# Optimization experiments

Measured on AMD Instinct MI355X. Metric: run time of the kernel, lower is better.

Reference implementation:

```python
import jax, jax.numpy as jnp
import numpy as np

B = 65536       # batch (rollout particles)
H = 5           # history_steps
F = 50          # forward_steps
DT = 0.01


def setup_inputs() -> dict:
    key = jax.random.key(0)
    k0, k1, k2, k3, k4, k5 = jax.random.split(key, 6)
    full_states = jax.random.uniform(k0, (B, H, 8), jnp.float32, 0.1, 1.0)
    actions = jax.random.uniform(k1, (B, F, 2), jnp.float32, 0.0, 0.5)
    fc1_w = jax.random.normal(k2, (16, 5 * H), jnp.float32) * 0.1
    fc1_b = jax.random.normal(k3, (16,), jnp.float32) * 0.1
    fc2_w = jax.random.normal(k4, (3, 16), jnp.float32) * 0.1
    fc2_b = jax.random.normal(k5, (3,), jnp.float32) * 0.1
    # [lf, lr, m_div_Iz, cm1, cm2, cr, cd, tire_B, tire_C, tire_D]
    params = jnp.array([0.09 - 0.036, 0.036, 0.05 * 12.0 / 0.02,
                        7.0, 0.1, 0.24 * 7.0, 0.1,
                        10.0, 0.1, (180.0 / np.pi) / 10.0 / 0.1], jnp.float32)
    return {"full_states": full_states, "actions": actions,
            "fc1_w": fc1_w, "fc1_b": fc1_b, "fc2_w": fc2_w, "fc2_b": fc2_b,
            "params": params, "enable_rnn": 1}


def reference(full_states, actions, fc1_w, fc1_b, fc2_w, fc2_b, params, enable_rnn):
    lf, lr, m_div_Iz = params[0], params[1], params[2]
    cm1, cm2, cr, cd = params[3], params[4], params[5], params[6]
    tB, tC, tD = params[7], params[8], params[9]
    bounds = jnp.array([5.0, 5.0, 3.0], full_states.dtype)
    dt = jnp.asarray(DT, full_states.dtype)
    pi = jnp.asarray(np.pi, full_states.dtype)

    def tire(slip):  # Pacejka magic formula
        return tD * jnp.sin(tC * jnp.arctan(tB * slip))

    def step(window, action):
        # window: [B, H, 8] rolling history of full states; action: [B, 2]
        latest = window[:, -1, :]
        throttle, steering = latest[:, 6], latest[:, 7]
        psi = latest[:, 4]
        c, s = jnp.cos(psi), jnp.sin(psi)
        # world -> body frame velocities (omega forced to 0 as in source)
        Vx = latest[:, 1] * c + latest[:, 3] * s
        Vy = -latest[:, 1] * s + latest[:, 3] * c
        slip_f = -jnp.arctan(Vy / Vx) + steering
        slip_r = jnp.arctan(-Vy / Vx)
        laf, lar = tire(slip_f), tire(slip_r)
        fwd_acc = (cm1 - cm2 * Vx) * throttle - cr - cd * Vx * Vx
        Vx = Vx + (fwd_acc - laf * jnp.sin(steering)) * dt
        Vy = Vy + (lar + laf * jnp.cos(steering)) * dt
        omega = m_div_Iz * (laf * lf * jnp.cos(steering) - lar * lr) * dt
        if enable_rnn:
            ph = window[:, :, 4]
            ch, sh = jnp.cos(ph), jnp.sin(ph)
            Vxh = window[:, :, 1] * ch + window[:, :, 3] * sh
            Vyh = -window[:, :, 1] * sh + window[:, :, 3] * ch
            # stack order matches torch.stack([Vx,Vy,omega,throttle,steering],dim=1).view(B,-1)
            feat = jnp.concatenate([Vxh, Vyh, window[:, :, 5],
                                    window[:, :, 6], window[:, :, 7]], axis=1)  # [B, 5H]
            y1 = jnp.tanh(feat @ fc1_w.T + fc1_b)
            y2 = jnp.tanh(y1 @ fc2_w.T + fc2_b) * bounds
            Vx = Vx + y2[:, 0] * dt
            Vy = Vy + y2[:, 1] * dt
            omega = omega + y2[:, 2] * dt
        # body -> world frame
        Vxg = Vx * c - Vy * s
        Vyg = Vx * s + Vy * c
        psi_new = jnp.mod(psi + omega * dt + pi, 2 * pi) - pi
        new_state = jnp.stack([latest[:, 0] + Vxg * dt, Vxg,
                               latest[:, 2] + Vyg * dt, Vyg,
                               psi_new, omega], axis=1)          # [B, 6]
        new_full = jnp.concatenate([new_state, action], axis=1)   # [B, 8]
        window = jnp.concatenate([window[:, 1:], new_full[:, None]], axis=1)
        return window, new_full

    _, outs = jax.lax.scan(step, full_states, jnp.swapaxes(actions, 0, 1))
    return jnp.swapaxes(outs, 0, 1)  # [B, F, 8] = future_states
```

## Files before the change

### kernel.cpp

```cpp
#include <hip/hip_runtime.h>
#include <hip/hip_fp16.h>
#include <math.h>


__device__ __forceinline__ float rfl(float x) {
    return __int_as_float(__builtin_amdgcn_readfirstlane(__float_as_int(x)));
}

__device__ __forceinline__ float mixlo(unsigned int w, float f, float acc) {
    float d;
    asm("v_fma_mix_f32 %0, %1, %2, %3 op_sel:[0,0,0] op_sel_hi:[1,0,0]"
        : "=v"(d) : "v"(w), "v"(f), "v"(acc));
    return d;
}
__device__ __forceinline__ float mixhi(unsigned int w, float f, float acc) {
    float d;
    asm("v_fma_mix_f32 %0, %1, %2, %3 op_sel:[1,0,0] op_sel_hi:[1,0,0]"
        : "=v"(d) : "v"(w), "v"(f), "v"(acc));
    return d;
}

__device__ __forceinline__ float fast_tanhf(float x) {
    float e = __builtin_amdgcn_exp2f(x * 2.8853900817779268f);
    return 1.0f - 2.0f * __builtin_amdgcn_rcpf(e + 1.0f);
}

__device__ __forceinline__ float sin_small(float x) {
    float x2 = x * x;
    return x * (1.0f + x2 * (-1.66666667e-1f + x2 * 8.33333338e-3f));
}

__device__ __forceinline__ float fatanf(float x) {
    float ax = fabsf(x);
    bool big = ax > 1.0f;
    float z  = big ? __builtin_amdgcn_rcpf(ax) : ax;
    float z2 = z * z;
    float p = fmaf(z2, -0.0117212f, 0.05265332f);
    p = fmaf(z2, p, -0.11643287f);
    p = fmaf(z2, p,  0.19354346f);
    p = fmaf(z2, p, -0.33262347f);
    p = fmaf(z2, p,  0.99997726f);
    float r = z * p;
    r = big ? (1.57079632679489662f - r) : r;
    return copysignf(r, x);
}

#define FOR_K_TAIL(M) \
    M(1) M(2) M(3) M(4) M(5) M(6) M(7) M(8) M(9) M(10) M(11) M(12) \
    M(13) M(14) M(15) M(16) M(17) M(18) M(19) M(20) M(21) M(22) M(23) M(24)
#define FOR_K_ALL(M) M(0) FOR_K_TAIL(M)

__global__ __launch_bounds__(256)
__attribute__((amdgpu_waves_per_eu(1, 1)))
void sim_kernel(const float* __restrict__ fs,
                const float* __restrict__ act,
                const float* __restrict__ w1,
                const float* __restrict__ b1,
                const float* __restrict__ w2,
                const float* __restrict__ b2,
                const float* __restrict__ prm,
                const int*   __restrict__ rnnp,
                float* __restrict__ out)
{
    __shared__ unsigned int sWH[200];

    const int tid = threadIdx.x;
    if (tid < 200) {
        int k = tid >> 3, j = tid & 7;
        unsigned int lo = (unsigned int)__half_as_ushort(__float2half(w1[(2 * j) * 25 + k]));
        unsigned int hi = (unsigned int)__half_as_ushort(__float2half(w1[(2 * j + 1) * 25 + k]));
        sWH[tid] = lo | (hi << 16);
    }
    __syncthreads();

    const int b = blockIdx.x * 256 + tid;

    const float4* fsp = reinterpret_cast<const float4*>(fs + (size_t)b * 40);
    const float4* ap  = reinterpret_cast<const float4*>(act + (size_t)b * 100);
    float4 acur = ap[0];

    float wf[40];
#pragma unroll
    for (int i = 0; i < 10; ++i) {
        float4 v = fsp[i];
        wf[i * 4 + 0] = v.x; wf[i * 4 + 1] = v.y;
        wf[i * 4 + 2] = v.z; wf[i * 4 + 3] = v.w;
    }

    const float lf = rfl(prm[0]), lr = rfl(prm[1]), mIz = rfl(prm[2]);
    const float cm1 = rfl(prm[3]), cm2 = rfl(prm[4]), cr = rfl(prm[5]);
    const float cd = rfl(prm[6]);
    const float tB = rfl(prm[7]), tC = rfl(prm[8]), tD = rfl(prm[9]);
    const int   rnn = __builtin_amdgcn_readfirstlane(rnnp[0]);
    const float dt = 0.01f;
    const float PI = 3.14159265358979323846f;
    const float INV2PI = 0.15915494309189535f;
    const float TWOPI = 6.28318530717958647692f;

#define DECLW2(K) \
    float w2a_##K = rfl(w2[(K)]);      \
    float w2b_##K = rfl(w2[16 + (K)]); \
    float w2c_##K = rfl(w2[32 + (K)]);
    DECLW2(0) DECLW2(1) DECLW2(2) DECLW2(3)
    DECLW2(4) DECLW2(5) DECLW2(6) DECLW2(7)
    DECLW2(8) DECLW2(9) DECLW2(10) DECLW2(11)
    DECLW2(12) DECLW2(13) DECLW2(14) DECLW2(15)
#undef DECLW2
    const float b2s0 = rfl(b2[0]), b2s1 = rfl(b2[1]), b2s2 = rfl(b2[2]);

#define DECLB1(K) float b1v_##K = b1[(K)];
    DECLB1(0) DECLB1(1) DECLB1(2) DECLB1(3)
    DECLB1(4) DECLB1(5) DECLB1(6) DECLB1(7)
    DECLB1(8) DECLB1(9) DECLB1(10) DECLB1(11)
    DECLB1(12) DECLB1(13) DECLB1(14) DECLB1(15)
#undef DECLB1

    float feat[25];
#pragma unroll
    for (int t = 0; t < 5; ++t) {
        float ph = wf[t * 8 + 4];
        float ch = __cosf(ph), sh = __sinf(ph);
        float v1 = wf[t * 8 + 1], v3 = wf[t * 8 + 3];
        feat[t]      =  v1 * ch + v3 * sh;
        feat[5 + t]  = -v1 * sh + v3 * ch;
        feat[10 + t] = wf[t * 8 + 5];
        feat[15 + t] = wf[t * 8 + 6];
        feat[20 + t] = wf[t * 8 + 7];
    }

    float x   = wf[32];
    float y   = wf[34];
    float psi = wf[36];
    float c = __cosf(psi), s = __sinf(psi);

#define WLOAD(K)                                                             \
    unsigned int wp##K##_0, wp##K##_1, wp##K##_2, wp##K##_3,                 \
                 wp##K##_4, wp##K##_5, wp##K##_6, wp##K##_7;                 \
    {                                                                        \
        const uint4* p = reinterpret_cast<const uint4*>(&sWH[(K) * 8]);      \
        uint4 u0 = p[0], u1 = p[1];                                          \
        wp##K##_0 = u0.x; wp##K##_1 = u0.y;                                  \
        wp##K##_2 = u0.z; wp##K##_3 = u0.w;                                  \
        wp##K##_4 = u1.x; wp##K##_5 = u1.y;                                  \
        wp##K##_6 = u1.z; wp##K##_7 = u1.w;                                  \
    }
    FOR_K_ALL(WLOAD)
#undef WLOAD

    float* outp = out + (size_t)b * 400;

#pragma unroll 1
    for (int f2 = 0; f2 < 25; ++f2) {
        float4 anext = ap[(f2 < 24) ? (f2 + 1) : 24];

#pragma unroll
        for (int half = 0; half < 2; ++half) {
            const float a0 = half ? acur.z : acur.x;
            const float a1 = half ? acur.w : acur.y;

            const float throttle = feat[19];
            const float steering = feat[24];
            const float Vx = feat[4];
            const float Vy = feat[9];

            const float atr    = fatanf(Vy * __builtin_amdgcn_rcpf(Vx));
            const float slip_f = -atr + steering;
            const float slip_r = -atr;
            const float laf = tD * sin_small(tC * fatanf(tB * slip_f));
            const float lar = tD * sin_small(tC * fatanf(tB * slip_r));

            const float st_s = __sinf(steering), st_c = __cosf(steering);
            const float fwd  = (cm1 - cm2 * Vx) * throttle - cr - cd * Vx * Vx;

            float Vx2   = Vx + (fwd - laf * st_s) * dt;
            float Vy2   = Vy + (lar + laf * st_c) * dt;
            float omega = mIz * (laf * lf * st_c - lar * lr) * dt;

            if (rnn) {
                const float f0 = feat[0];
                float y1_0  = mixlo(wp0_0, f0, b1v_0);
                float y1_1  = mixhi(wp0_0, f0, b1v_1);
                float y1_2  = mixlo(wp0_1, f0, b1v_2);
                float y1_3  = mixhi(wp0_1, f0, b1v_3);
                float y1_4  = mixlo(wp0_2, f0, b1v_4);
                float y1_5  = mixhi(wp0_2, f0, b1v_5);
                float y1_6  = mixlo(wp0_3, f0, b1v_6);
                float y1_7  = mixhi(wp0_3, f0, b1v_7);
                float y1_8  = mixlo(wp0_4, f0, b1v_8);
                float y1_9  = mixhi(wp0_4, f0, b1v_9);
                float y1_10 = mixlo(wp0_5, f0, b1v_10);
                float y1_11 = mixhi(wp0_5, f0, b1v_11);
                float y1_12 = mixlo(wp0_6, f0, b1v_12);
                float y1_13 = mixhi(wp0_6, f0, b1v_13);
                float y1_14 = mixlo(wp0_7, f0, b1v_14);
                float y1_15 = mixhi(wp0_7, f0, b1v_15);
#define GK(K)                                        \
                {                                    \
                    const float fk = feat[(K)];      \
                    y1_0  = mixlo(wp##K##_0, fk, y1_0);  \
                    y1_1  = mixhi(wp##K##_0, fk, y1_1);  \
                    y1_2  = mixlo(wp##K##_1, fk, y1_2);  \
                    y1_3  = mixhi(wp##K##_1, fk, y1_3);  \
                    y1_4  = mixlo(wp##K##_2, fk, y1_4);  \
                    y1_5  = mixhi(wp##K##_2, fk, y1_5);  \
                    y1_6  = mixlo(wp##K##_3, fk, y1_6);  \
                    y1_7  = mixhi(wp##K##_3, fk, y1_7);  \
                    y1_8  = mixlo(wp##K##_4, fk, y1_8);  \
                    y1_9  = mixhi(wp##K##_4, fk, y1_9);  \
                    y1_10 = mixlo(wp##K##_5, fk, y1_10); \
                    y1_11 = mixhi(wp##K##_5, fk, y1_11); \
                    y1_12 = mixlo(wp##K##_6, fk, y1_12); \
                    y1_13 = mixhi(wp##K##_6, fk, y1_13); \
                    y1_14 = mixlo(wp##K##_7, fk, y1_14); \
                    y1_15 = mixhi(wp##K##_7, fk, y1_15); \
                }
                FOR_K_TAIL(GK)
#undef GK

                float z0 = b2s0, z1 = b2s1, z2 = b2s2;
#define FC2(K)                                       \
                {                                    \
                    float t_ = fast_tanhf(y1_##K);   \
                    z0 = fmaf(t_, w2a_##K, z0);      \
                    z1 = fmaf(t_, w2b_##K, z1);      \
                    z2 = fmaf(t_, w2c_##K, z2);      \
                }
                FC2(0) FC2(1) FC2(2) FC2(3)
                FC2(4) FC2(5) FC2(6) FC2(7)
                FC2(8) FC2(9) FC2(10) FC2(11)
                FC2(12) FC2(13) FC2(14) FC2(15)
#undef FC2
                Vx2   += fast_tanhf(z0) * 5.0f * dt;
                Vy2   += fast_tanhf(z1) * 5.0f * dt;
                omega += fast_tanhf(z2) * 3.0f * dt;
            }

            const float Vxg = Vx2 * c - Vy2 * s;
            const float Vyg = Vx2 * s + Vy2 * c;
            float pn = psi + omega * dt + PI;
            pn = pn - floorf(pn * INV2PI) * TWOPI - PI;

            x = x + Vxg * dt;
            y = y + Vyg * dt;

            float4 o0 = make_float4(x, Vxg, y, Vyg);
            float4 o1 = make_float4(pn, omega, a0, a1);
            reinterpret_cast<float4*>(outp)[0] = o0;
            reinterpret_cast<float4*>(outp)[1] = o1;
            outp += 8;

            psi = pn;
            c = __cosf(pn);
            s = __sinf(pn);
#pragma unroll
            for (int j = 0; j < 5; ++j)
#pragma unroll
                for (int t = 0; t < 4; ++t)
                    feat[j * 5 + t] = feat[j * 5 + t + 1];
            feat[4]  =  Vxg * c + Vyg * s;
            feat[9]  = -Vxg * s + Vyg * c;
            feat[14] = omega;
            feat[19] = a0;
            feat[24] = a1;
        }
        acur = anext;
    }
}

extern "C" void kernel_launch(void* const* d_in, const int* in_sizes, int n_in,
                              void* d_out, int out_size, void* d_ws, size_t ws_size,
                              hipStream_t stream) {
    const float* fs  = (const float*)d_in[0];
    const float* act = (const float*)d_in[1];
    const float* w1  = (const float*)d_in[2];
    const float* b1  = (const float*)d_in[3];
    const float* w2  = (const float*)d_in[4];
    const float* b2  = (const float*)d_in[5];
    const float* prm = (const float*)d_in[6];
    const int*   rnn = (const int*)d_in[7];
    float* out = (float*)d_out;

    const int Bn = in_sizes[0] / 40;
    dim3 grid(Bn / 256), block(256);
    hipLaunchKernelGGL(sim_kernel, grid, block, 0, stream,
                       fs, act, w1, b1, w2, b2, prm, rnn, out);
}
```

Baseline: 213.5 us.

## Split each car across two lanes, halving MLP hidden units per lane

Each car is now handled by a pair of adjacent lanes. Each lane computes 8 of the 16 hidden units of the first MLP layer and a partial second-layer sum, and the partials are combined with a cross-lane shuffle. Each lane also writes one float4 half of the output row. Both lanes duplicate the scalar physics. The grid doubles, the waves-per-EU hint rises to 2, and the accumulating fma_mix calls now use read-write asm operands. The aim is lower register pressure and more parallelism on the serial rollout, at the cost of redundant physics work and a shuffle every step.

New measurement: 206.8 us. -3.1%, faster.

```diff
diff --git a/kernel.cpp b/kernel.cpp
--- a/kernel.cpp
+++ b/kernel.cpp
@@ -7,16 +7,24 @@
     return __int_as_float(__builtin_amdgcn_readfirstlane(__float_as_int(x)));
 }
 
-__device__ __forceinline__ float mixlo(unsigned int w, float f, float acc) {
+__device__ __forceinline__ void mixlo_acc(float& acc, unsigned int w, float f) {
+    asm("v_fma_mix_f32 %0, %1, %2, %0 op_sel:[0,0,0] op_sel_hi:[1,0,0]"
+        : "+v"(acc) : "v"(w), "v"(f));
+}
+__device__ __forceinline__ void mixhi_acc(float& acc, unsigned int w, float f) {
+    asm("v_fma_mix_f32 %0, %1, %2, %0 op_sel:[1,0,0] op_sel_hi:[1,0,0]"
+        : "+v"(acc) : "v"(w), "v"(f));
+}
+__device__ __forceinline__ float mixlo_init(unsigned int w, float f, float c) {
     float d;
     asm("v_fma_mix_f32 %0, %1, %2, %3 op_sel:[0,0,0] op_sel_hi:[1,0,0]"
-        : "=v"(d) : "v"(w), "v"(f), "v"(acc));
+        : "=v"(d) : "v"(w), "v"(f), "v"(c));
     return d;
 }
-__device__ __forceinline__ float mixhi(unsigned int w, float f, float acc) {
+__device__ __forceinline__ float mixhi_init(unsigned int w, float f, float c) {
     float d;
     asm("v_fma_mix_f32 %0, %1, %2, %3 op_sel:[1,0,0] op_sel_hi:[1,0,0]"
-        : "=v"(d) : "v"(w), "v"(f), "v"(acc));
+        : "=v"(d) : "v"(w), "v"(f), "v"(c));
     return d;
 }
 
@@ -51,7 +59,7 @@
 #define FOR_K_ALL(M) M(0) FOR_K_TAIL(M)
 
 __global__ __launch_bounds__(256)
-__attribute__((amdgpu_waves_per_eu(1, 1)))
+__attribute__((amdgpu_waves_per_eu(2, 2)))
 void sim_kernel(const float* __restrict__ fs,
                 const float* __restrict__ act,
                 const float* __restrict__ w1,
@@ -73,10 +81,12 @@
     }
     __syncthreads();
 
-    const int b = blockIdx.x * 256 + tid;
-
-    const float4* fsp = reinterpret_cast<const float4*>(fs + (size_t)b * 40);
-    const float4* ap  = reinterpret_cast<const float4*>(act + (size_t)b * 100);
+    const int gt  = blockIdx.x * 256 + tid;
+    const int car = gt >> 1;
+    const int h   = gt & 1;
+
+    const float4* fsp = reinterpret_cast<const float4*>(fs + (size_t)car * 40);
+    const float4* ap  = reinterpret_cast<const float4*>(act + (size_t)car * 100);
     float4 acur = ap[0];
 
     float wf[40];
@@ -96,24 +106,32 @@
     const float PI = 3.14159265358979323846f;
     const float INV2PI = 0.15915494309189535f;
     const float TWOPI = 6.28318530717958647692f;
-
-#define DECLW2(K) \
-    float w2a_##K = rfl(w2[(K)]);      \
-    float w2b_##K = rfl(w2[16 + (K)]); \
-    float w2c_##K = rfl(w2[32 + (K)]);
-    DECLW2(0) DECLW2(1) DECLW2(2) DECLW2(3)
-    DECLW2(4) DECLW2(5) DECLW2(6) DECLW2(7)
-    DECLW2(8) DECLW2(9) DECLW2(10) DECLW2(11)
-    DECLW2(12) DECLW2(13) DECLW2(14) DECLW2(15)
-#undef DECLW2
     const float b2s0 = rfl(b2[0]), b2s1 = rfl(b2[1]), b2s2 = rfl(b2[2]);
 
-#define DECLB1(K) float b1v_##K = b1[(K)];
-    DECLB1(0) DECLB1(1) DECLB1(2) DECLB1(3)
-    DECLB1(4) DECLB1(5) DECLB1(6) DECLB1(7)
-    DECLB1(8) DECLB1(9) DECLB1(10) DECLB1(11)
-    DECLB1(12) DECLB1(13) DECLB1(14) DECLB1(15)
-#undef DECLB1
+    float b1v_0, b1v_1, b1v_2, b1v_3, b1v_4, b1v_5, b1v_6, b1v_7;
+    {
+        const float4* p = reinterpret_cast<const float4*>(b1 + 8 * h);
+        float4 u0 = p[0], u1 = p[1];
+        b1v_0 = u0.x; b1v_1 = u0.y; b1v_2 = u0.z; b1v_3 = u0.w;
+        b1v_4 = u1.x; b1v_5 = u1.y; b1v_6 = u1.z; b1v_7 = u1.w;
+    }
+    float w2av_0, w2av_1, w2av_2, w2av_3, w2av_4, w2av_5, w2av_6, w2av_7;
+    float w2bv_0, w2bv_1, w2bv_2, w2bv_3, w2bv_4, w2bv_5, w2bv_6, w2bv_7;
+    float w2cv_0, w2cv_1, w2cv_2, w2cv_3, w2cv_4, w2cv_5, w2cv_6, w2cv_7;
+    {
+        const float4* pa = reinterpret_cast<const float4*>(w2 + 8 * h);
+        float4 a0_ = pa[0], a1_ = pa[1];
+        w2av_0 = a0_.x; w2av_1 = a0_.y; w2av_2 = a0_.z; w2av_3 = a0_.w;
+        w2av_4 = a1_.x; w2av_5 = a1_.y; w2av_6 = a1_.z; w2av_7 = a1_.w;
+        const float4* pb = reinterpret_cast<const float4*>(w2 + 16 + 8 * h);
+        float4 b0_ = pb[0], b1_ = pb[1];
+        w2bv_0 = b0_.x; w2bv_1 = b0_.y; w2bv_2 = b0_.z; w2bv_3 = b0_.w;
+        w2bv_4 = b1_.x; w2bv_5 = b1_.y; w2bv_6 = b1_.z; w2bv_7 = b1_.w;
+        const float4* pc = reinterpret_cast<const float4*>(w2 + 32 + 8 * h);
+        float4 c0_ = pc[0], c1_ = pc[1];
+        w2cv_0 = c0_.x; w2cv_1 = c0_.y; w2cv_2 = c0_.z; w2cv_3 = c0_.w;
+        w2cv_4 = c1_.x; w2cv_5 = c1_.y; w2cv_6 = c1_.z; w2cv_7 = c1_.w;
+    }
 
     float feat[25];
 #pragma unroll
@@ -134,20 +152,17 @@
     float c = __cosf(psi), s = __sinf(psi);
 
 #define WLOAD(K)                                                             \
-    unsigned int wp##K##_0, wp##K##_1, wp##K##_2, wp##K##_3,                 \
-                 wp##K##_4, wp##K##_5, wp##K##_6, wp##K##_7;                 \
+    unsigned int wp##K##_0, wp##K##_1, wp##K##_2, wp##K##_3;                 \
     {                                                                        \
-        const uint4* p = reinterpret_cast<const uint4*>(&sWH[(K) * 8]);      \
-        uint4 u0 = p[0], u1 = p[1];                                          \
-        wp##K##_0 = u0.x; wp##K##_1 = u0.y;                                  \
-        wp##K##_2 = u0.z; wp##K##_3 = u0.w;                                  \
-        wp##K##_4 = u1.x; wp##K##_5 = u1.y;                                  \
-        wp##K##_6 = u1.z; wp##K##_7 = u1.w;                                  \
+        const uint4* p =                                                     \
+            reinterpret_cast<const uint4*>(&sWH[(K) * 8 + 4 * h]);           \
+        uint4 u = *p;                                                        \
+        wp##K##_0 = u.x; wp##K##_1 = u.y; wp##K##_2 = u.z; wp##K##_3 = u.w;  \
     }
     FOR_K_ALL(WLOAD)
 #undef WLOAD
 
-    float* outp = out + (size_t)b * 400;
+    float* outp = out + (size_t)car * 400 + 4 * h;
 
 #pragma unroll 1
     for (int f2 = 0; f2 < 25; ++f2) {
@@ -178,61 +193,47 @@
 
             if (rnn) {
                 const float f0 = feat[0];
-                float y1_0  = mixlo(wp0_0, f0, b1v_0);
-                float y1_1  = mixhi(wp0_0, f0, b1v_1);
-                float y1_2  = mixlo(wp0_1, f0, b1v_2);
-                float y1_3  = mixhi(wp0_1, f0, b1v_3);
-                float y1_4  = mixlo(wp0_2, f0, b1v_4);
-                float y1_5  = mixhi(wp0_2, f0, b1v_5);
-                float y1_6  = mixlo(wp0_3, f0, b1v_6);
-                float y1_7  = mixhi(wp0_3, f0, b1v_7);
-                float y1_8  = mixlo(wp0_4, f0, b1v_8);
-                float y1_9  = mixhi(wp0_4, f0, b1v_9);
-                float y1_10 = mixlo(wp0_5, f0, b1v_10);
-                float y1_11 = mixhi(wp0_5, f0, b1v_11);
-                float y1_12 = mixlo(wp0_6, f0, b1v_12);
-                float y1_13 = mixhi(wp0_6, f0, b1v_13);
-                float y1_14 = mixlo(wp0_7, f0, b1v_14);
-                float y1_15 = mixhi(wp0_7, f0, b1v_15);
-#define GK(K)                                        \
-                {                                    \
-                    const float fk = feat[(K)];      \
-                    y1_0  = mixlo(wp##K##_0, fk, y1_0);  \
-                    y1_1  = mixhi(wp##K##_0, fk, y1_1);  \
-                    y1_2  = mixlo(wp##K##_1, fk, y1_2);  \
-                    y1_3  = mixhi(wp##K##_1, fk, y1_3);  \
-                    y1_4  = mixlo(wp##K##_2, fk, y1_4);  \
-                    y1_5  = mixhi(wp##K##_2, fk, y1_5);  \
-                    y1_6  = mixlo(wp##K##_3, fk, y1_6);  \
-                    y1_7  = mixhi(wp##K##_3, fk, y1_7);  \
-                    y1_8  = mixlo(wp##K##_4, fk, y1_8);  \
-                    y1_9  = mixhi(wp##K##_4, fk, y1_9);  \
-                    y1_10 = mixlo(wp##K##_5, fk, y1_10); \
-                    y1_11 = mixhi(wp##K##_5, fk, y1_11); \
-                    y1_12 = mixlo(wp##K##_6, fk, y1_12); \
-                    y1_13 = mixhi(wp##K##_6, fk, y1_13); \
-                    y1_14 = mixlo(wp##K##_7, fk, y1_14); \
-                    y1_15 = mixhi(wp##K##_7, fk, y1_15); \
+                float y1_0 = mixlo_init(wp0_0, f0, b1v_0);
+                float y1_1 = mixhi_init(wp0_0, f0, b1v_1);
+                float y1_2 = mixlo_init(wp0_1, f0, b1v_2);
+                float y1_3 = mixhi_init(wp0_1, f0, b1v_3);
+                float y1_4 = mixlo_init(wp0_2, f0, b1v_4);
+                float y1_5 = mixhi_init(wp0_2, f0, b1v_5);
+                float y1_6 = mixlo_init(wp0_3, f0, b1v_6);
+                float y1_7 = mixhi_init(wp0_3, f0, b1v_7);
+#define GK(K)                                                \
+                {                                            \
+                    const float fk = feat[(K)];              \
+                    mixlo_acc(y1_0, wp##K##_0, fk);          \
+                    mixhi_acc(y1_1, wp##K##_0, fk);          \
+                    mixlo_acc(y1_2, wp##K##_1, fk);          \
+                    mixhi_acc(y1_3, wp##K##_1, fk);          \
+                    mixlo_acc(y1_4, wp##K##_2, fk);          \
+                    mixhi_acc(y1_5, wp##K##_2, fk);          \
+                    mixlo_acc(y1_6, wp##K##_3, fk);          \
+                    mixhi_acc(y1_7, wp##K##_3, fk);          \
                 }
                 FOR_K_TAIL(GK)
 #undef GK
 
-                float z0 = b2s0, z1 = b2s1, z2 = b2s2;
-#define FC2(K)                                       \
-                {                                    \
-                    float t_ = fast_tanhf(y1_##K);   \
-                    z0 = fmaf(t_, w2a_##K, z0);      \
-                    z1 = fmaf(t_, w2b_##K, z1);      \
-                    z2 = fmaf(t_, w2c_##K, z2);      \
+                float p0 = 0.0f, p1 = 0.0f, p2 = 0.0f;
+#define FC2(I)                                         \
+                {                                      \
+                    float t_ = fast_tanhf(y1_##I);     \
+                    p0 = fmaf(t_, w2av_##I, p0);       \
+                    p1 = fmaf(t_, w2bv_##I, p1);       \
+                    p2 = fmaf(t_, w2cv_##I, p2);       \
                 }
                 FC2(0) FC2(1) FC2(2) FC2(3)
                 FC2(4) FC2(5) FC2(6) FC2(7)
-                FC2(8) FC2(9) FC2(10) FC2(11)
-                FC2(12) FC2(13) FC2(14) FC2(15)
 #undef FC2
-                Vx2   += fast_tanhf(z0) * 5.0f * dt;
-                Vy2   += fast_tanhf(z1) * 5.0f * dt;
-                omega += fast_tanhf(z2) * 3.0f * dt;
+                p0 += __shfl_xor(p0, 1, 64);
+                p1 += __shfl_xor(p1, 1, 64);
+                p2 += __shfl_xor(p2, 1, 64);
+
+                Vx2   += fast_tanhf(b2s0 + p0) * 5.0f * dt;
+                Vy2   += fast_tanhf(b2s1 + p1) * 5.0f * dt;
+                omega += fast_tanhf(b2s2 + p2) * 3.0f * dt;
             }
 
             const float Vxg = Vx2 * c - Vy2 * s;
@@ -243,10 +244,12 @@
             x = x + Vxg * dt;
             y = y + Vyg * dt;
 
-            float4 o0 = make_float4(x, Vxg, y, Vyg);
-            float4 o1 = make_float4(pn, omega, a0, a1);
-            reinterpret_cast<float4*>(outp)[0] = o0;
-            reinterpret_cast<float4*>(outp)[1] = o1;
+            float4 ov;
+            ov.x = h ? pn    : x;
+            ov.y = h ? omega : Vxg;
+            ov.z = h ? a0    : y;
+            ov.w = h ? a1    : Vyg;
+            *reinterpret_cast<float4*>(outp) = ov;
             outp += 8;
 
             psi = pn;
@@ -281,7 +284,7 @@
     float* out = (float*)d_out;
 
     const int Bn = in_sizes[0] / 40;
-    dim3 grid(Bn / 256), block(256);
+    dim3 grid(Bn / 128), block(256);
     hipLaunchKernelGGL(sim_kernel, grid, block, 0, stream,
                        fs, act, w1, b1, w2, b2, prm, rnn, out);
 }
```
